# Kernel optimization log

Measured on AMD Instinct MI355X. Metric: run time of the kernel, lower is better.

The kernel has to match this reference:

```python
import jax, jax.numpy as jnp
import numpy as np

MAX_CH = 21
LAT_DIM = 64
D_EMBED = 1024
N_HEADS = 16
D_HEAD = D_EMBED // N_HEADS  # 64
L = MAX_CH * LAT_DIM         # 1344 latents
B, T = 4, 1024


def setup_inputs() -> dict:
    key = jax.random.key(0)
    k1, k2, k3, k4, k5, k6 = jax.random.split(key, 6)
    x = jax.random.normal(k1, (B, T, D_EMBED), dtype=jnp.float32)
    # boolean channel mask [b, L, T]
    ch_mask = jax.random.randint(k2, (B, L, T), 0, 2) > 0
    # learned latent queries [L, H*d] (xavier-uniform-ish init)
    lim_q = float(np.sqrt(6.0 / (L + N_HEADS * D_HEAD)))
    latent_q = jax.random.uniform(k3, (L, N_HEADS * D_HEAD), minval=-lim_q, maxval=lim_q, dtype=jnp.float32)
    # Linear weights (torch layout: [out, in]) and biases
    lim_w = float(np.sqrt(1.0 / D_EMBED))
    w_k_w = jax.random.uniform(k4, (N_HEADS * D_HEAD, D_EMBED), minval=-lim_w, maxval=lim_w, dtype=jnp.float32)
    w_k_b = jnp.zeros((N_HEADS * D_HEAD,), dtype=jnp.float32)
    w_v_w = jax.random.uniform(k5, (N_HEADS * D_HEAD, D_EMBED), minval=-lim_w, maxval=lim_w, dtype=jnp.float32)
    w_v_b = jax.random.uniform(k6, (N_HEADS * D_HEAD,), minval=-lim_w, maxval=lim_w, dtype=jnp.float32)
    return {"x": x, "ch_mask": ch_mask, "latent_q": latent_q,
            "w_k_w": w_k_w, "w_k_b": w_k_b, "w_v_w": w_v_w, "w_v_b": w_v_b}


def reference(x, ch_mask, latent_q, w_k_w, w_k_b, w_v_w, w_v_b):
    b, t, d = x.shape
    H, dh = N_HEADS, D_HEAD
    l = latent_q.shape[0]
    # faithful to torch .view(-1, H, L, d): raw row-major reinterpretation
    lq = latent_q.reshape(1, H, l, dh)                    # [1,H,L,dh]
    k = (x @ w_k_w.T + w_k_b).reshape(b, t, H, dh).transpose(0, 2, 3, 1)  # [b,H,dh,T]
    v = (x @ w_v_w.T + w_v_b).reshape(b, t, H, dh).transpose(0, 2, 1, 3)  # [b,H,T,dh]
    scale = jnp.float32(H) ** -0.5  # note: n_heads**-0.5, as in source
    scores = jnp.einsum('ohld,bhdt->bhlt', lq, k) * scale  # [b,H,L,T]
    mask = ch_mask[:, None, :, :]                           # [b,1,L,T] broadcast over heads
    scores = jnp.where(mask, scores, jnp.float32(-1e9))
    w = jax.nn.softmax(scores, axis=-1)
    w = jnp.where(mask, w, jnp.float32(0.0))
    out = jnp.einsum('bhlt,bhtd->bhld', w, v)               # [b,H,L,dh]
    return out.transpose(0, 2, 1, 3).reshape(b, l, H * dh)  # [b,L,H*dh]
```

## Files before the change

### kernel.cpp

```cpp
#include <hip/hip_runtime.h>
#include <hip/hip_bf16.h>

#define B_SZ 4
#define T_SZ 1024
#define NH 16
#define L_SZ 1344
#define LT_COUNT 21

typedef __attribute__((ext_vector_type(8))) short short8;
typedef __attribute__((ext_vector_type(4))) short short4v;
typedef __attribute__((ext_vector_type(4))) float floatx4;

typedef __attribute__((address_space(1))) const void gvoid;
typedef __attribute__((address_space(3))) void svoid;
#define GLD16(gp, lp) \
  __builtin_amdgcn_global_load_lds((gvoid*)(gp), (svoid*)(lp), 16, 0, 0)

static __device__ inline short bf16bits(float f) {
  return __builtin_bit_cast(short, __float2bfloat16(f));
}
static __device__ inline short4v cvt4(float4 v) {
  short4v r;
  r.x = bf16bits(v.x); r.y = bf16bits(v.y);
  r.z = bf16bits(v.z); r.w = bf16bits(v.w);
  return r;
}

static __device__ inline unsigned pack_bf16_2(float a, float b) {
  unsigned ua = __builtin_bit_cast(unsigned, a) + 0x8000u;
  unsigned ub = __builtin_bit_cast(unsigned, b) + 0x8000u;
  return __builtin_amdgcn_perm(ub, ua, 0x07060302u);
}
static __device__ inline uint2 pack_bf16_4(float4 v) {
  return make_uint2(pack_bf16_2(v.x, v.y), pack_bf16_2(v.z, v.w));
}


__global__ __launch_bounds__(256) void mask_detect(
    const unsigned char* __restrict__ m, int* __restrict__ flag) {
  __shared__ int any_off4, any_at4;
  if (threadIdx.x == 0) { any_off4 = 0; any_at4 = 0; }
  __syncthreads();
  int a1 = 0, a2 = 0;
  for (int i = threadIdx.x; i < 4096; i += 256) {
    unsigned char v = m[i];
    if (v) {
      if ((i & 3) != 0) a1 = 1;
      if ((i & 7) == 4) a2 = 1;
    }
  }
  if (a1) atomicOr(&any_off4, 1);
  if (a2) atomicOr(&any_at4, 1);
  __syncthreads();
  if (threadIdx.x == 0) *flag = any_off4 ? 1 : (any_at4 ? 0 : 2);
}

__global__ __launch_bounds__(256) void maskbits_kernel(
    const void* __restrict__ mask, const int* __restrict__ flag,
    unsigned int* __restrict__ bits) {
  int idx = blockIdx.x * 256 + threadIdx.x;
  int f = *flag;
  bool v;
  if (f == 1)      v = ((const signed char*)mask)[idx] != 0;
  else if (f == 2) v = ((const long long*)mask)[idx] != 0;
  else             v = ((const int*)mask)[idx] != 0;
  unsigned long long bal = __ballot(v);
  int lane = threadIdx.x & 63;
  if ((lane & 31) == 0) {
    unsigned int w = (lane & 32) ? (unsigned int)(bal >> 32) : (unsigned int)bal;
    bits[idx >> 5] = w;
  }
}

__global__ __launch_bounds__(256) void cvt_bf16(
    const float4* __restrict__ src, uint2* __restrict__ dst) {
  size_t i = (size_t)blockIdx.x * 256 + threadIdx.x;
  dst[i] = pack_bf16_4(src[i]);
}

static __device__ __forceinline__ void epi_k(const floatx4 acc[4][4],
    int bxt, int byd, int wm, int wn, int c15, int kq,
    const float* __restrict__ bk, __hip_bfloat16* __restrict__ k_buf) {
  #pragma unroll
  for (int ni = 0; ni < 4; ++ni) {
    int gr = bxt * 128 + wn * 64 + ni * 16 + c15;
    int b = gr >> 10, tc = (gr >> 6) & 15;
    #pragma unroll
    for (int mi = 0; mi < 4; ++mi) {
      int d0 = byd * 128 + wm * 64 + mi * 16 + kq * 4;
      int h = d0 >> 6, hd = d0 & 63;
      int half = hd >> 5, q4 = (hd >> 3) & 3, jlo = hd & 7;
      int bh = b * 16 + h;
      float4 b4 = *(const float4*)(bk + d0);
      float4 v4 = {acc[mi][ni][0] + b4.x, acc[mi][ni][1] + b4.y,
                   acc[mi][ni][2] + b4.z, acc[mi][ni][3] + b4.w};
      *(uint2*)(k_buf + ((size_t)((bh * 16 + tc) * 8 + ni * 2 + half)) * 512 +
                (q4 * 16 + c15) * 8 + jlo) = pack_bf16_4(v4);
    }
  }
}

static __device__ __forceinline__ void epi_v(const floatx4 acc[4][4],
    int bxd, int byt, int wm, int wn, int c15, int kq,
    const float* __restrict__ bv, __hip_bfloat16* __restrict__ v_buf) {
  #pragma unroll
  for (int ni = 0; ni < 4; ++ni) {
    int d = bxd * 128 + wn * 64 + ni * 16 + c15;
    int h = d >> 6;
    float bias = bv[d];
    #pragma unroll
    for (int mi = 0; mi < 4; ++mi) {
      int gr = byt * 128 + wm * 64 + mi * 16 + kq * 4;
      int b = gr >> 10, tc = (gr >> 6) & 15;
      int tl = gr & 63;
      int half = tl >> 5, q4 = (tl >> 3) & 3, jlo = tl & 7;
      int bh = b * 16 + h;
      float4 v4 = {acc[mi][ni][0] + bias, acc[mi][ni][1] + bias,
                   acc[mi][ni][2] + bias, acc[mi][ni][3] + bias};
      *(uint2*)(v_buf + ((size_t)((bh * 16 + tc) * 8 + ni * 2 + half)) * 512 +
                (q4 * 16 + c15) * 8 + jlo) = pack_bf16_4(v4);
    }
  }
}

static __device__ __forceinline__ void gemm_core(
    const __hip_bfloat16* __restrict__ A, const __hip_bfloat16* __restrict__ B,
    __hip_bfloat16* ldsA, __hip_bfloat16* ldsB,
    int TA, int TB, int tid, floatx4 (&acc)[4][4]) {
  const int lane = tid & 63, w = tid >> 6;
  const int wm = w & 1, wn = w >> 1;
  const int c15 = lane & 15, kq = lane >> 4;
  for (int kk = 0; kk < 1024; kk += 32) {
    #pragma unroll
    for (int j = 0; j < 2; ++j) {
      int c = w * 128 + j * 64 + lane;
      int row = c >> 2;
      int gkc = (c & 3) ^ (row & 3);
      GLD16(A + (size_t)(TA * 128 + row) * 1024 + kk + gkc * 8,
            ldsA + (w * 128 + j * 64) * 8);
      GLD16(B + (size_t)(TB * 128 + row) * 1024 + kk + gkc * 8,
            ldsB + (w * 128 + j * 64) * 8);
    }
    __syncthreads();
    short8 af[4], bf[4];
    #pragma unroll
    for (int mi = 0; mi < 4; ++mi) {
      int row = wm * 64 + mi * 16 + c15;
      af[mi] = *(const short8*)(ldsA + row * 32 + ((kq ^ (row & 3)) * 8));
    }
    #pragma unroll
    for (int ni = 0; ni < 4; ++ni) {
      int row = wn * 64 + ni * 16 + c15;
      bf[ni] = *(const short8*)(ldsB + row * 32 + ((kq ^ (row & 3)) * 8));
    }
    #pragma unroll
    for (int mi = 0; mi < 4; ++mi)
      #pragma unroll
      for (int ni = 0; ni < 4; ++ni)
        acc[mi][ni] = __builtin_amdgcn_mfma_f32_16x16x32_bf16(
            af[mi], bf[ni], acc[mi][ni], 0, 0, 0);
    __syncthreads();
  }
}

__global__ __launch_bounds__(256) void gemm_kv_bf16(
    const __hip_bfloat16* __restrict__ xb,
    const __hip_bfloat16* __restrict__ wkb, const __hip_bfloat16* __restrict__ wvb,
    const float* __restrict__ bk, const float* __restrict__ bv,
    __hip_bfloat16* __restrict__ k_buf, __hip_bfloat16* __restrict__ v_buf) {
  __shared__ __align__(16) __hip_bfloat16 ldsA[128 * 32];
  __shared__ __align__(16) __hip_bfloat16 ldsB[128 * 32];
  const int tid = threadIdx.x;
  const int lane = tid & 63, w = tid >> 6;
  const int wm = w & 1, wn = w >> 1;
  const int c15 = lane & 15, kq = lane >> 4;
  floatx4 acc[4][4];
  for (int i = 0; i < 4; ++i)
    for (int j = 0; j < 4; ++j) acc[i][j] = (floatx4){0.f, 0.f, 0.f, 0.f};

  if (blockIdx.z == 0) {
    gemm_core(wkb, xb, ldsA, ldsB, blockIdx.y, blockIdx.x, tid, acc);
    epi_k(acc, blockIdx.x, blockIdx.y, wm, wn, c15, kq, bk, k_buf);
  } else {
    gemm_core(xb, wvb, ldsA, ldsB, blockIdx.x, blockIdx.y, tid, acc);
    epi_v(acc, blockIdx.y, blockIdx.x, wm, wn, c15, kq, bv, v_buf);
  }
}

__global__ __launch_bounds__(64, 2) void attn_kernel(
    const float* __restrict__ latent_q,
    const __hip_bfloat16* __restrict__ k_buf,
    const __hip_bfloat16* __restrict__ v_buf,
    const unsigned int* __restrict__ mbits,
    float* __restrict__ out) {
  __shared__ __align__(16) __hip_bfloat16 pbuf[4][16 * 72];
  __shared__ uint2 mrows[64][17];

  const int lane = threadIdx.x & 63;
  int bid = blockIdx.x;
  int xcd = bid & 7, j = bid >> 3;
  int bh = xcd * 8 + j / LT_COUNT;
  int lt = j % LT_COUNT;
  int h = bh & 15, b = bh >> 4;
  const int q4 = lane >> 4, c15 = lane & 15;
  const int l0 = lt * 64;

  {
    const unsigned int* msrc = mbits + (size_t)(b * L_SZ + l0) * 32;
    #pragma unroll
    for (int p = 0; p < 8; ++p) {
      int i = p * 64 + lane;
      uint4 m4 = *(const uint4*)(msrc + i * 4);
      int row = i >> 3, c2 = (i & 7) * 2;
      mrows[row][c2]     = make_uint2(m4.x, m4.y);
      mrows[row][c2 + 1] = make_uint2(m4.z, m4.w);
    }
  }

  const float QS = 0.25f * 1.44269504089f;
  short8 qf[4][2];
  #pragma unroll
  for (int g = 0; g < 4; ++g) {
    const float* qp = latent_q + ((size_t)(h * L_SZ + l0 + g * 16 + c15)) * 64 + q4 * 8;
    float4 a0 = *(const float4*)(qp);
    float4 a1 = *(const float4*)(qp + 4);
    float4 a2 = *(const float4*)(qp + 32);
    float4 a3 = *(const float4*)(qp + 36);
    a0.x *= QS; a0.y *= QS; a0.z *= QS; a0.w *= QS;
    a1.x *= QS; a1.y *= QS; a1.z *= QS; a1.w *= QS;
    a2.x *= QS; a2.y *= QS; a2.z *= QS; a2.w *= QS;
    a3.x *= QS; a3.y *= QS; a3.z *= QS; a3.w *= QS;
    short4v t0 = cvt4(a0), t1 = cvt4(a1), t2 = cvt4(a2), t3 = cvt4(a3);
    qf[g][0] = (short8){t0.x, t0.y, t0.z, t0.w, t1.x, t1.y, t1.z, t1.w};
    qf[g][1] = (short8){t2.x, t2.y, t2.z, t2.w, t3.x, t3.y, t3.z, t3.w};
  }

  floatx4 l4[4];
  floatx4 o_acc[4][4];
  #pragma unroll
  for (int g = 0; g < 4; ++g) {
    l4[g] = (floatx4){0.f, 0.f, 0.f, 0.f};
    #pragma unroll
    for (int di = 0; di < 4; ++di) o_acc[g][di] = (floatx4){0.f, 0.f, 0.f, 0.f};
  }

  const __hip_bfloat16* kb = k_buf + (size_t)bh * 65536;
  const __hip_bfloat16* vb = v_buf + (size_t)bh * 65536;

  for (int tc = 0; tc < 16; ++tc) {
    short8 kf[2][4], vf[2][4];
    #pragma unroll
    for (int half = 0; half < 2; ++half)
      #pragma unroll
      for (int ni = 0; ni < 4; ++ni)
        kf[half][ni] = *(const short8*)(kb + (size_t)(tc * 8 + ni * 2 + half) * 512 + lane * 8);
    #pragma unroll
    for (int half = 0; half < 2; ++half)
      #pragma unroll
      for (int di = 0; di < 4; ++di)
        vf[half][di] = *(const short8*)(vb + (size_t)(tc * 8 + di * 2 + half) * 512 + lane * 8);

    #pragma unroll
    for (int g = 0; g < 4; ++g) {
      uint2 mw = mrows[g * 16 + c15][tc];
      floatx4 s[4];
      #pragma unroll
      for (int ni = 0; ni < 4; ++ni) s[ni] = (floatx4){0.f, 0.f, 0.f, 0.f};
      #pragma unroll
      for (int half = 0; half < 2; ++half)
        #pragma unroll
        for (int ni = 0; ni < 4; ++ni)
          s[ni] = __builtin_amdgcn_mfma_f32_16x16x32_bf16(kf[half][ni], qf[g][half], s[ni], 0, 0, 0);
      __hip_bfloat16* pw = pbuf[g];
      #pragma unroll
      for (int ni = 0; ni < 4; ++ni) {
        unsigned mword = (ni >= 2) ? mw.y : mw.x;
        float4 p4;
        #pragma unroll
        for (int r = 0; r < 4; ++r) {
          float e = exp2f(s[ni][r]);
          int sh = (ni & 1) * 16 + q4 * 4 + r;
          ((float*)&p4)[r] = ((mword >> sh) & 1) ? e : 0.f;
        }
        l4[g][0] += p4.x; l4[g][1] += p4.y;
        l4[g][2] += p4.z; l4[g][3] += p4.w;
        *(uint2*)(pw + c15 * 72 + ni * 16 + q4 * 4) = pack_bf16_4(p4);
      }
    }

    #pragma unroll
    for (int g = 0; g < 4; ++g) {
      short8 pf0 = *(const short8*)(pbuf[g] + c15 * 72 + q4 * 8);
      short8 pf1 = *(const short8*)(pbuf[g] + c15 * 72 + 32 + q4 * 8);
      #pragma unroll
      for (int di = 0; di < 4; ++di)
        o_acc[g][di] = __builtin_amdgcn_mfma_f32_16x16x32_bf16(vf[0][di], pf0, o_acc[g][di], 0, 0, 0);
      #pragma unroll
      for (int di = 0; di < 4; ++di)
        o_acc[g][di] = __builtin_amdgcn_mfma_f32_16x16x32_bf16(vf[1][di], pf1, o_acc[g][di], 0, 0, 0);
    }
  }

  #pragma unroll
  for (int g = 0; g < 4; ++g) {
    float la = (l4[g][0] + l4[g][1]) + (l4[g][2] + l4[g][3]);
    la += __shfl_xor(la, 16, 64);
    la += __shfl_xor(la, 32, 64);
    float inv = (la > 0.f) ? 1.f / la : 0.f;
    float* ob = out + ((size_t)(b * L_SZ + l0 + g * 16 + c15)) * 1024 + h * 64;
    #pragma unroll
    for (int di = 0; di < 4; ++di) {
      float4 o4 = {o_acc[g][di][0] * inv, o_acc[g][di][1] * inv,
                   o_acc[g][di][2] * inv, o_acc[g][di][3] * inv};
      *(float4*)(ob + di * 16 + q4 * 4) = o4;
    }
  }
}

extern "C" void kernel_launch(void* const* d_in, const int* in_sizes, int n_in,
                              void* d_out, int out_size, void* d_ws, size_t ws_size,
                              hipStream_t stream) {
  const float* x      = (const float*)d_in[0];
  const void* ch_mask = d_in[1];
  const float* lq     = (const float*)d_in[2];
  const float* wk     = (const float*)d_in[3];
  const float* bk     = (const float*)d_in[4];
  const float* wv     = (const float*)d_in[5];
  const float* bv     = (const float*)d_in[6];
  float* out = (float*)d_out;

  char* ws = (char*)d_ws;
  unsigned int* mbits   = (unsigned int*)ws;
  int* flag             = (int*)(ws + 720896);
  __hip_bfloat16* k_buf = (__hip_bfloat16*)(ws + 786432);
  __hip_bfloat16* v_buf = (__hip_bfloat16*)(ws + 786432 + 8388608);

  __hip_bfloat16* xb  = (__hip_bfloat16*)d_out;
  __hip_bfloat16* wkb = xb + 4 * 1024 * 1024;
  __hip_bfloat16* wvb = wkb + 1024 * 1024;

  mask_detect<<<1, 256, 0, stream>>>((const unsigned char*)ch_mask, flag);
  maskbits_kernel<<<21504, 256, 0, stream>>>(ch_mask, flag, mbits);

  cvt_bf16<<<4096, 256, 0, stream>>>((const float4*)x, (uint2*)xb);
  cvt_bf16<<<1024, 256, 0, stream>>>((const float4*)wk, (uint2*)wkb);
  cvt_bf16<<<1024, 256, 0, stream>>>((const float4*)wv, (uint2*)wvb);
  gemm_kv_bf16<<<dim3(32, 8, 2), 256, 0, stream>>>(xb, wkb, wvb, bk, bv, k_buf, v_buf);

  attn_kernel<<<8 * 168, 64, 0, stream>>>(lq, k_buf, v_buf, mbits, out);
}
```

Measured before the change: 216.3 us.

## Split attention over two T halves with fp16 partials and combine pass

Splits the attention over the token dimension into two halves, doubling the block count to raise occupancy on the machine (1344 single-wave blocks before). Each half writes fp16 partial outputs interleaved into the output buffer plus fp32 row sums, and a combine kernel sums and normalizes them in place. The three fp32-to-bf16 conversion launches are also merged into one. This adds an extra pass over the output and fp16 rounding of the partials, and it only runs when the workspace is large enough.

```diff
diff --git a/kernel.cpp b/kernel.cpp
--- a/kernel.cpp
+++ b/kernel.cpp
@@ -1,11 +1,13 @@
 #include <hip/hip_runtime.h>
 #include <hip/hip_bf16.h>
+#include <hip/hip_fp16.h>
 
 #define B_SZ 4
 #define T_SZ 1024
 #define NH 16
 #define L_SZ 1344
 #define LT_COUNT 21
+#define NROWS 86016
 
 typedef __attribute__((ext_vector_type(8))) short short8;
 typedef __attribute__((ext_vector_type(4))) short short4v;
@@ -72,10 +74,16 @@
   }
 }
 
-__global__ __launch_bounds__(256) void cvt_bf16(
-    const float4* __restrict__ src, uint2* __restrict__ dst) {
-  size_t i = (size_t)blockIdx.x * 256 + threadIdx.x;
-  dst[i] = pack_bf16_4(src[i]);
+__global__ __launch_bounds__(256) void cvt_all(
+    const float4* __restrict__ x, const float4* __restrict__ wk,
+    const float4* __restrict__ wv,
+    uint2* __restrict__ xb, uint2* __restrict__ wkb, uint2* __restrict__ wvb) {
+  int bidx = blockIdx.x;
+  const float4* s; uint2* d; size_t i;
+  if (bidx < 4096)      { s = x;  d = xb;  i = (size_t)bidx * 256 + threadIdx.x; }
+  else if (bidx < 5120) { s = wk; d = wkb; i = (size_t)(bidx - 4096) * 256 + threadIdx.x; }
+  else                  { s = wv; d = wvb; i = (size_t)(bidx - 5120) * 256 + threadIdx.x; }
+  d[i] = pack_bf16_4(s[i]);
 }
 
 static __device__ __forceinline__ void epi_k(const floatx4 acc[4][4],
@@ -187,38 +195,10 @@
   }
 }
 
-__global__ __launch_bounds__(64, 2) void attn_kernel(
-    const float* __restrict__ latent_q,
-    const __hip_bfloat16* __restrict__ k_buf,
-    const __hip_bfloat16* __restrict__ v_buf,
-    const unsigned int* __restrict__ mbits,
-    float* __restrict__ out) {
-  __shared__ __align__(16) __hip_bfloat16 pbuf[4][16 * 72];
-  __shared__ uint2 mrows[64][17];
-
-  const int lane = threadIdx.x & 63;
-  int bid = blockIdx.x;
-  int xcd = bid & 7, j = bid >> 3;
-  int bh = xcd * 8 + j / LT_COUNT;
-  int lt = j % LT_COUNT;
-  int h = bh & 15, b = bh >> 4;
-  const int q4 = lane >> 4, c15 = lane & 15;
-  const int l0 = lt * 64;
-
-  {
-    const unsigned int* msrc = mbits + (size_t)(b * L_SZ + l0) * 32;
-    #pragma unroll
-    for (int p = 0; p < 8; ++p) {
-      int i = p * 64 + lane;
-      uint4 m4 = *(const uint4*)(msrc + i * 4);
-      int row = i >> 3, c2 = (i & 7) * 2;
-      mrows[row][c2]     = make_uint2(m4.x, m4.y);
-      mrows[row][c2 + 1] = make_uint2(m4.z, m4.w);
-    }
-  }
-
+static __device__ __forceinline__ void load_qfrags(
+    const float* __restrict__ latent_q, int h, int l0, int c15, int q4,
+    short8 (&qf)[4][2]) {
   const float QS = 0.25f * 1.44269504089f;
-  short8 qf[4][2];
   #pragma unroll
   for (int g = 0; g < 4; ++g) {
     const float* qp = latent_q + ((size_t)(h * L_SZ + l0 + g * 16 + c15)) * 64 + q4 * 8;
@@ -234,6 +214,43 @@
     qf[g][0] = (short8){t0.x, t0.y, t0.z, t0.w, t1.x, t1.y, t1.z, t1.w};
     qf[g][1] = (short8){t2.x, t2.y, t2.z, t2.w, t3.x, t3.y, t3.z, t3.w};
   }
+}
+
+__global__ __launch_bounds__(64, 4) void attn_split(
+    const float* __restrict__ latent_q,
+    const __hip_bfloat16* __restrict__ k_buf,
+    const __hip_bfloat16* __restrict__ v_buf,
+    const unsigned int* __restrict__ mbits,
+    __half* __restrict__ part,
+    float* __restrict__ lpart) {
+  __shared__ __align__(16) __hip_bfloat16 pbuf[4][16 * 72];
+  __shared__ uint2 mrows[64][9];
+
+  const int lane = threadIdx.x & 63;
+  int bid = blockIdx.x;
+  int xcd = bid & 7, j = bid >> 3;
+  int half = j / 168, j2 = j % 168;
+  int bh = xcd * 8 + j2 / LT_COUNT;
+  int lt = j2 % LT_COUNT;
+  int h = bh & 15, b = bh >> 4;
+  const int q4 = lane >> 4, c15 = lane & 15;
+  const int l0 = lt * 64;
+  const int tc0 = half * 8;
+
+  {
+    const unsigned int* msrc = mbits + (size_t)(b * L_SZ + l0) * 32 + half * 16;
+    #pragma unroll
+    for (int p = 0; p < 4; ++p) {
+      int i = p * 64 + lane;
+      int row = i >> 2, ch = i & 3;
+      uint4 m4 = *(const uint4*)(msrc + (size_t)row * 32 + ch * 4);
+      mrows[row][ch * 2]     = make_uint2(m4.x, m4.y);
+      mrows[row][ch * 2 + 1] = make_uint2(m4.z, m4.w);
+    }
+  }
+
+  short8 qf[4][2];
+  load_qfrags(latent_q, h, l0, c15, q4, qf);
 
   floatx4 l4[4];
   floatx4 o_acc[4][4];
@@ -247,30 +264,31 @@
   const __hip_bfloat16* kb = k_buf + (size_t)bh * 65536;
   const __hip_bfloat16* vb = v_buf + (size_t)bh * 65536;
 
-  for (int tc = 0; tc < 16; ++tc) {
+  for (int tcl = 0; tcl < 8; ++tcl) {
+    int tc = tc0 + tcl;
     short8 kf[2][4], vf[2][4];
     #pragma unroll
-    for (int half = 0; half < 2; ++half)
+    for (int hf = 0; hf < 2; ++hf)
       #pragma unroll
       for (int ni = 0; ni < 4; ++ni)
-        kf[half][ni] = *(const short8*)(kb + (size_t)(tc * 8 + ni * 2 + half) * 512 + lane * 8);
-    #pragma unroll
-    for (int half = 0; half < 2; ++half)
+        kf[hf][ni] = *(const short8*)(kb + (size_t)(tc * 8 + ni * 2 + hf) * 512 + lane * 8);
+    #pragma unroll
+    for (int hf = 0; hf < 2; ++hf)
       #pragma unroll
       for (int di = 0; di < 4; ++di)
-        vf[half][di] = *(const short8*)(vb + (size_t)(tc * 8 + di * 2 + half) * 512 + lane * 8);
+        vf[hf][di] = *(const short8*)(vb + (size_t)(tc * 8 + di * 2 + hf) * 512 + lane * 8);
 
     #pragma unroll
     for (int g = 0; g < 4; ++g) {
-      uint2 mw = mrows[g * 16 + c15][tc];
+      uint2 mw = mrows[g * 16 + c15][tcl];
       floatx4 s[4];
       #pragma unroll
       for (int ni = 0; ni < 4; ++ni) s[ni] = (floatx4){0.f, 0.f, 0.f, 0.f};
       #pragma unroll
-      for (int half = 0; half < 2; ++half)
+      for (int hf = 0; hf < 2; ++hf)
         #pragma unroll
         for (int ni = 0; ni < 4; ++ni)
-          s[ni] = __builtin_amdgcn_mfma_f32_16x16x32_bf16(kf[half][ni], qf[g][half], s[ni], 0, 0, 0);
+          s[ni] = __builtin_amdgcn_mfma_f32_16x16x32_bf16(kf[hf][ni], qf[g][hf], s[ni], 0, 0, 0);
       __hip_bfloat16* pw = pbuf[g];
       #pragma unroll
       for (int ni = 0; ni < 4; ++ni) {
@@ -306,6 +324,137 @@
     float la = (l4[g][0] + l4[g][1]) + (l4[g][2] + l4[g][3]);
     la += __shfl_xor(la, 16, 64);
     la += __shfl_xor(la, 32, 64);
+    int row = (b * L_SZ + l0 + g * 16 + c15) * 16 + h;
+    if (lane < 16) lpart[half * NROWS + row] = la;
+    size_t ebase = (size_t)row * 64;
+    #pragma unroll
+    for (int di = 0; di < 4; ++di)
+      #pragma unroll
+      for (int r = 0; r < 4; ++r) {
+        size_t e = ebase + di * 16 + q4 * 4 + r;
+        part[2 * e + half] = __float2half(o_acc[g][di][r]);
+      }
+  }
+}
+
+__global__ __launch_bounds__(256) void combine_kernel(
+    unsigned long long* __restrict__ buf, const float* __restrict__ lpart) {
+  size_t i = (size_t)blockIdx.x * 256 + threadIdx.x;
+  unsigned long long w = buf[i];
+  int row = (int)((2 * i) >> 6);
+  float l = lpart[row] + lpart[NROWS + row];
+  float inv = (l > 0.f) ? 1.f / l : 0.f;
+  __half2 a = __builtin_bit_cast(__half2, (unsigned)(w & 0xFFFFFFFFull));
+  __half2 c = __builtin_bit_cast(__half2, (unsigned)(w >> 32));
+  float2 o = {(__half2float(a.x) + __half2float(a.y)) * inv,
+              (__half2float(c.x) + __half2float(c.y)) * inv};
+  buf[i] = __builtin_bit_cast(unsigned long long, o);
+}
+
+__global__ __launch_bounds__(64, 2) void attn_kernel(
+    const float* __restrict__ latent_q,
+    const __hip_bfloat16* __restrict__ k_buf,
+    const __hip_bfloat16* __restrict__ v_buf,
+    const unsigned int* __restrict__ mbits,
+    float* __restrict__ out) {
+  __shared__ __align__(16) __hip_bfloat16 pbuf[4][16 * 72];
+  __shared__ uint2 mrows[64][17];
+
+  const int lane = threadIdx.x & 63;
+  int bid = blockIdx.x;
+  int xcd = bid & 7, j = bid >> 3;
+  int bh = xcd * 8 + j / LT_COUNT;
+  int lt = j % LT_COUNT;
+  int h = bh & 15, b = bh >> 4;
+  const int q4 = lane >> 4, c15 = lane & 15;
+  const int l0 = lt * 64;
+
+  {
+    const unsigned int* msrc = mbits + (size_t)(b * L_SZ + l0) * 32;
+    #pragma unroll
+    for (int p = 0; p < 8; ++p) {
+      int i = p * 64 + lane;
+      uint4 m4 = *(const uint4*)(msrc + i * 4);
+      int row = i >> 3, c2 = (i & 7) * 2;
+      mrows[row][c2]     = make_uint2(m4.x, m4.y);
+      mrows[row][c2 + 1] = make_uint2(m4.z, m4.w);
+    }
+  }
+
+  short8 qf[4][2];
+  load_qfrags(latent_q, h, l0, c15, q4, qf);
+
+  floatx4 l4[4];
+  floatx4 o_acc[4][4];
+  #pragma unroll
+  for (int g = 0; g < 4; ++g) {
+    l4[g] = (floatx4){0.f, 0.f, 0.f, 0.f};
+    #pragma unroll
+    for (int di = 0; di < 4; ++di) o_acc[g][di] = (floatx4){0.f, 0.f, 0.f, 0.f};
+  }
+
+  const __hip_bfloat16* kb = k_buf + (size_t)bh * 65536;
+  const __hip_bfloat16* vb = v_buf + (size_t)bh * 65536;
+
+  for (int tc = 0; tc < 16; ++tc) {
+    short8 kf[2][4], vf[2][4];
+    #pragma unroll
+    for (int hf = 0; hf < 2; ++hf)
+      #pragma unroll
+      for (int ni = 0; ni < 4; ++ni)
+        kf[hf][ni] = *(const short8*)(kb + (size_t)(tc * 8 + ni * 2 + hf) * 512 + lane * 8);
+    #pragma unroll
+    for (int hf = 0; hf < 2; ++hf)
+      #pragma unroll
+      for (int di = 0; di < 4; ++di)
+        vf[hf][di] = *(const short8*)(vb + (size_t)(tc * 8 + di * 2 + hf) * 512 + lane * 8);
+
+    #pragma unroll
+    for (int g = 0; g < 4; ++g) {
+      uint2 mw = mrows[g * 16 + c15][tc];
+      floatx4 s[4];
+      #pragma unroll
+      for (int ni = 0; ni < 4; ++ni) s[ni] = (floatx4){0.f, 0.f, 0.f, 0.f};
+      #pragma unroll
+      for (int hf = 0; hf < 2; ++hf)
+        #pragma unroll
+        for (int ni = 0; ni < 4; ++ni)
+          s[ni] = __builtin_amdgcn_mfma_f32_16x16x32_bf16(kf[hf][ni], qf[g][hf], s[ni], 0, 0, 0);
+      __hip_bfloat16* pw = pbuf[g];
+      #pragma unroll
+      for (int ni = 0; ni < 4; ++ni) {
+        unsigned mword = (ni >= 2) ? mw.y : mw.x;
+        float4 p4;
+        #pragma unroll
+        for (int r = 0; r < 4; ++r) {
+          float e = exp2f(s[ni][r]);
+          int sh = (ni & 1) * 16 + q4 * 4 + r;
+          ((float*)&p4)[r] = ((mword >> sh) & 1) ? e : 0.f;
+        }
+        l4[g][0] += p4.x; l4[g][1] += p4.y;
+        l4[g][2] += p4.z; l4[g][3] += p4.w;
+        *(uint2*)(pw + c15 * 72 + ni * 16 + q4 * 4) = pack_bf16_4(p4);
+      }
+    }
+
+    #pragma unroll
+    for (int g = 0; g < 4; ++g) {
+      short8 pf0 = *(const short8*)(pbuf[g] + c15 * 72 + q4 * 8);
+      short8 pf1 = *(const short8*)(pbuf[g] + c15 * 72 + 32 + q4 * 8);
+      #pragma unroll
+      for (int di = 0; di < 4; ++di)
+        o_acc[g][di] = __builtin_amdgcn_mfma_f32_16x16x32_bf16(vf[0][di], pf0, o_acc[g][di], 0, 0, 0);
+      #pragma unroll
+      for (int di = 0; di < 4; ++di)
+        o_acc[g][di] = __builtin_amdgcn_mfma_f32_16x16x32_bf16(vf[1][di], pf1, o_acc[g][di], 0, 0, 0);
+    }
+  }
+
+  #pragma unroll
+  for (int g = 0; g < 4; ++g) {
+    float la = (l4[g][0] + l4[g][1]) + (l4[g][2] + l4[g][3]);
+    la += __shfl_xor(la, 16, 64);
+    la += __shfl_xor(la, 32, 64);
     float inv = (la > 0.f) ? 1.f / la : 0.f;
     float* ob = out + ((size_t)(b * L_SZ + l0 + g * 16 + c15)) * 1024 + h * 64;
     #pragma unroll
@@ -334,6 +483,8 @@
   int* flag             = (int*)(ws + 720896);
   __hip_bfloat16* k_buf = (__hip_bfloat16*)(ws + 786432);
   __hip_bfloat16* v_buf = (__hip_bfloat16*)(ws + 786432 + 8388608);
+  float* lpart          = (float*)(ws + 17563648);
+  const bool can_split = ws_size >= 18251776ull;
 
   __hip_bfloat16* xb  = (__hip_bfloat16*)d_out;
   __hip_bfloat16* wkb = xb + 4 * 1024 * 1024;
@@ -341,11 +492,16 @@
 
   mask_detect<<<1, 256, 0, stream>>>((const unsigned char*)ch_mask, flag);
   maskbits_kernel<<<21504, 256, 0, stream>>>(ch_mask, flag, mbits);
-
-  cvt_bf16<<<4096, 256, 0, stream>>>((const float4*)x, (uint2*)xb);
-  cvt_bf16<<<1024, 256, 0, stream>>>((const float4*)wk, (uint2*)wkb);
-  cvt_bf16<<<1024, 256, 0, stream>>>((const float4*)wv, (uint2*)wvb);
+  cvt_all<<<6144, 256, 0, stream>>>((const float4*)x, (const float4*)wk,
+                                    (const float4*)wv,
+                                    (uint2*)xb, (uint2*)wkb, (uint2*)wvb);
   gemm_kv_bf16<<<dim3(32, 8, 2), 256, 0, stream>>>(xb, wkb, wvb, bk, bv, k_buf, v_buf);
 
-  attn_kernel<<<8 * 168, 64, 0, stream>>>(lq, k_buf, v_buf, mbits, out);
-}
+  if (can_split) {
+    attn_split<<<8 * 336, 64, 0, stream>>>(lq, k_buf, v_buf, mbits,
+                                           (__half*)d_out, lpart);
+    combine_kernel<<<10752, 256, 0, stream>>>((unsigned long long*)d_out, lpart);
+  } else {
+    attn_kernel<<<8 * 168, 64, 0, stream>>>(lq, k_buf, v_buf, mbits, out);
+  }
+}
```

Measured after the change: 221.7 us. +2.5%, slower.
